# Performance work log

Measured on AMD Instinct MI355X. Metric: run time of the kernel, lower is better.

## Reference

```python
import jax, jax.numpy as jnp
import numpy as np

M, K = 8192, 4096
N_INT4, N_INT8 = 8192, 2816
N_TOTAL = N_INT4 + N_INT8


def setup_inputs() -> dict:
    key = jax.random.key(0)
    k1, k2, k3, k4, k5 = jax.random.split(key, 5)
    x = jax.random.normal(k1, (M, K), dtype=jnp.float32)
    # Precomputed dequantized weight buffers (what forward() actually consumes).
    # Scaled down ~1/sqrt(K) to keep activations O(1), mimicking dequantized int4/int8 weights.
    w_int4_deq = jax.random.normal(k2, (N_INT4, K), dtype=jnp.float32) * 0.02
    w_int8_deq = jax.random.normal(k3, (N_INT8, K), dtype=jnp.float32) * 0.02
    # inv_perm: random permutation mapping concatenated [int4|int8] channels back to original order
    inv_perm = jax.random.permutation(k4, N_TOTAL).astype(jnp.int64)
    bias = jax.random.normal(k5, (N_TOTAL,), dtype=jnp.float32)
    return {"x": x, "w_int4_deq": w_int4_deq, "w_int8_deq": w_int8_deq,
            "inv_perm": inv_perm, "bias": bias}


def reference(x, w_int4_deq, w_int8_deq, inv_perm, bias):
    # Two GEMMs on dequantized weight groups: y = x @ W^T
    y_int4 = jnp.einsum('mk,nk->mn', x, w_int4_deq)   # [M, N_int4]
    y_int8 = jnp.einsum('mk,nk->mn', x, w_int8_deq)   # [M, N_int8]
    y = jnp.concatenate([y_int4, y_int8], axis=-1)    # [M, N_total]
    # Output-channel permutation back to original layout, then bias add
    y = jnp.take(y, inv_perm, axis=-1) + bias
    return y
```

## Files before the change

### kernel.cpp

```cpp
#include <hip/hip_runtime.h>
#include <hip/hip_bf16.h>

#define M_DIM 8192
#define K_DIM 4096
#define N4    8192
#define N8    2816
#define NT    11008
#define TM    (M_DIM / 256)
#define TN    (NT / 256)
#define NKT   (K_DIM / 64)

typedef __attribute__((ext_vector_type(4))) float  f32x4;
typedef __attribute__((ext_vector_type(4))) float  float4v;
typedef __attribute__((ext_vector_type(8))) __bf16 bf16x8;
typedef __attribute__((ext_vector_type(4))) unsigned short ushort4v;
typedef __attribute__((ext_vector_type(8))) unsigned short ushort8v;

__device__ __forceinline__ unsigned short f2bf(float f) {
  union { float f; unsigned int u; } v; v.f = f;
  unsigned int u = v.u;
  unsigned int r = u + 0x7FFFu + ((u >> 16) & 1u);
  return (unsigned short)(r >> 16);
}

__global__ void conv_x_kernel(const float* __restrict__ x,
                              unsigned short* __restrict__ xb, int n8) {
  int idx = blockIdx.x * blockDim.x + threadIdx.x;
  int stride = gridDim.x * blockDim.x;
  for (int i = idx; i < n8; i += stride) {
    const float4v* src = (const float4v*)(x + (size_t)i * 8);
    float4v a = src[0], b = src[1];
    ushort8v o;
    o[0] = f2bf(a[0]); o[1] = f2bf(a[1]); o[2] = f2bf(a[2]); o[3] = f2bf(a[3]);
    o[4] = f2bf(b[0]); o[5] = f2bf(b[1]); o[6] = f2bf(b[2]); o[7] = f2bf(b[3]);
    ((ushort8v*)xb)[i] = o;
  }
}

__global__ void conv_w_kernel(const float* __restrict__ w4,
                              const float* __restrict__ w8,
                              const int* __restrict__ inv_perm,
                              unsigned short* __restrict__ wb) {
  int j = blockIdx.x;
  int c = inv_perm[j];
  const float* src = (c < N4) ? (w4 + (size_t)c * K_DIM)
                              : (w8 + (size_t)(c - N4) * K_DIM);
  unsigned short* dst = wb + (size_t)j * K_DIM;
  int t = threadIdx.x;
#pragma unroll
  for (int it = 0; it < 4; ++it) {
    int e = it * 1024 + t * 4;
    float4v a = *(const float4v*)(src + e);
    ushort4v o;
    o[0] = f2bf(a[0]); o[1] = f2bf(a[1]); o[2] = f2bf(a[2]); o[3] = f2bf(a[3]);
    *(ushort4v*)(dst + e) = o;
  }
}

__global__ __launch_bounds__(512, 2)
void gemm256_kernel(const unsigned short* __restrict__ A,
                    const unsigned short* __restrict__ B,
                    const float* __restrict__ bias,
                    float* __restrict__ C) {
  __shared__ __align__(16) unsigned short lds[4 * 16384];

  int bid = blockIdx.x;
  int wgid = (bid & 7) * ((TM * TN) / 8) + (bid >> 3);
  int tile_m = wgid / TN;
  int tile_n = wgid % TN;

  const int tid  = threadIdx.x;
  const int wid  = tid >> 6;
  const int lane = tid & 63;
  const int wr  = wid >> 2;
  const int wcn = wid & 3;
  const int l15 = lane & 15;
  const int rswz  = (lane & 7) << 4;
  const int coff0 = (((lane >> 4) * 16) + 0)  ^ rswz;
  const int coff1 = (((lane >> 4) * 16) + 64) ^ rswz;
  const int st_row8 = lane >> 3;
  const int st_scol = ((lane & 7) * 16) ^ ((lane & 0x38) << 1);

  const size_t arow0 = (size_t)tile_m * 256;
  const size_t brow0 = (size_t)tile_n * 256;

  auto stage = [&](const unsigned short* __restrict__ g, size_t grow0,
                   unsigned short* ltile, int q, int ktelem) {
    int row = q * 64 + wid * 8 + st_row8;
    const unsigned short* src =
        g + (grow0 + (size_t)row) * K_DIM + ktelem + (st_scol >> 1);
    unsigned short* dst = ltile + (q * 64 + wid * 8) * 64;
    __builtin_amdgcn_global_load_lds(
        (const __attribute__((address_space(1))) void*)src,
        (__attribute__((address_space(3))) void*)dst, 16, 0, 0);
  };
  auto fragld = [&](const unsigned short* ltile, int row, int coff) -> bf16x8 {
    return *(const bf16x8*)((const char*)ltile + row * 128 + coff);
  };

  f32x4 acc[8][4];
#pragma unroll
  for (int i = 0; i < 8; ++i)
#pragma unroll
    for (int j = 0; j < 4; ++j) acc[i][j] = (f32x4){0.f, 0.f, 0.f, 0.f};

  bf16x8 b0[2][2];


  stage(A, arow0, lds + 0,     0, 0);  stage(A, arow0, lds + 0,     2, 0);
  stage(A, arow0, lds + 0,     1, 0);  stage(A, arow0, lds + 0,     3, 0);
  stage(B, brow0, lds + 16384, 0, 0);  stage(B, brow0, lds + 16384, 1, 0);
  stage(B, brow0, lds + 16384, 2, 0);  stage(B, brow0, lds + 16384, 3, 0);
  stage(A, arow0, lds + 32768, 0, 64); stage(A, arow0, lds + 32768, 2, 64);
  stage(B, brow0, lds + 49152, 0, 64); stage(B, brow0, lds + 49152, 1, 64);
  stage(B, brow0, lds + 49152, 2, 64); stage(B, brow0, lds + 49152, 3, 64);
  asm volatile("s_waitcnt vmcnt(6)" ::: "memory");
  __builtin_amdgcn_s_barrier();

#pragma unroll
  for (int n = 0; n < 2; ++n) {
    int row = wcn * 64 + n * 16 + l15;
    b0[n][0] = fragld(lds + 16384, row, coff0);
    b0[n][1] = fragld(lds + 16384, row, coff1);
  }

#define KITER(AC, BC, AN, UN1, UN2)                                           \
  {                                                                           \
    unsigned short* const Ac = (AC);                                          \
    unsigned short* const Bc = (BC);                                          \
    unsigned short* const An = (AN);                                          \
    const int un1 = (UN1);                                                    \
    const int un2 = (UN2);                                                    \
    bf16x8 a0[4][2], a1[4][2], b1[2][2];                                      \
                \
    _Pragma("unroll")                                                         \
    for (int m = 0; m < 4; ++m) {                                             \
      int row = wr * 128 + m * 16 + l15;                                      \
      a0[m][0] = fragld(Ac, row, coff0);                                      \
      a0[m][1] = fragld(Ac, row, coff1);                                      \
    }                                                                         \
    stage(A, arow0, An, 1, un1);                                              \
    stage(A, arow0, An, 3, un1);                                              \
    __builtin_amdgcn_s_barrier();                                             \
    asm volatile("s_waitcnt lgkmcnt(0)" ::: "memory");                        \
    __builtin_amdgcn_sched_barrier(0);                                        \
    __builtin_amdgcn_s_setprio(1);                                            \
    _Pragma("unroll")                                                         \
    for (int m = 0; m < 4; ++m)                                               \
      _Pragma("unroll")                                                       \
      for (int n = 0; n < 2; ++n) {                                           \
        acc[m][n] = __builtin_amdgcn_mfma_f32_16x16x32_bf16(a0[m][0], b0[n][0], acc[m][n], 0, 0, 0); \
        acc[m][n] = __builtin_amdgcn_mfma_f32_16x16x32_bf16(a0[m][1], b0[n][1], acc[m][n], 0, 0, 0); \
      }                                                                       \
    __builtin_amdgcn_s_setprio(0);                                            \
    __builtin_amdgcn_s_barrier();                                             \
     \
    _Pragma("unroll")                                                         \
    for (int n = 0; n < 2; ++n) {                                             \
      int row = wcn * 64 + (2 + n) * 16 + l15;                                \
      b1[n][0] = fragld(Bc, row, coff0);                                      \
      b1[n][1] = fragld(Bc, row, coff1);                                      \
    }                                                                         \
    stage(A, arow0, Ac, 0, un2);                                              \
    stage(A, arow0, Ac, 2, un2);                                              \
    __builtin_amdgcn_s_barrier();                                             \
    asm volatile("s_waitcnt lgkmcnt(0)" ::: "memory");                        \
    __builtin_amdgcn_sched_barrier(0);                                        \
    __builtin_amdgcn_s_setprio(1);                                            \
    _Pragma("unroll")                                                         \
    for (int m = 0; m < 4; ++m)                                               \
      _Pragma("unroll")                                                       \
      for (int n = 0; n < 2; ++n) {                                           \
        acc[m][2 + n] = __builtin_amdgcn_mfma_f32_16x16x32_bf16(a0[m][0], b1[n][0], acc[m][2 + n], 0, 0, 0); \
        acc[m][2 + n] = __builtin_amdgcn_mfma_f32_16x16x32_bf16(a0[m][1], b1[n][1], acc[m][2 + n], 0, 0, 0); \
      }                                                                       \
    __builtin_amdgcn_s_setprio(0);                                            \
    asm volatile("s_waitcnt vmcnt(10)" ::: "memory");      \
    __builtin_amdgcn_s_barrier();                                             \
            \
    _Pragma("unroll")                                                         \
    for (int m = 0; m < 4; ++m) {                                             \
      int row = wr * 128 + 64 + m * 16 + l15;                                 \
      a1[m][0] = fragld(Ac, row, coff0);                                      \
      a1[m][1] = fragld(Ac, row, coff1);                                      \
    }                                                                         \
    stage(B, brow0, Bc, 0, un2);                                              \
    stage(B, brow0, Bc, 1, un2);                                              \
    __builtin_amdgcn_s_barrier();                                             \
    asm volatile("s_waitcnt lgkmcnt(0)" ::: "memory");                        \
    __builtin_amdgcn_sched_barrier(0);                                        \
    __builtin_amdgcn_s_setprio(1);                                            \
    _Pragma("unroll")                                                         \
    for (int m = 0; m < 4; ++m)                                               \
      _Pragma("unroll")                                                       \
      for (int n = 0; n < 2; ++n) {                                           \
        acc[4 + m][n] = __builtin_amdgcn_mfma_f32_16x16x32_bf16(a1[m][0], b0[n][0], acc[4 + m][n], 0, 0, 0); \
        acc[4 + m][n] = __builtin_amdgcn_mfma_f32_16x16x32_bf16(a1[m][1], b0[n][1], acc[4 + m][n], 0, 0, 0); \
      }                                                                       \
    __builtin_amdgcn_s_setprio(0);                                            \
    __builtin_amdgcn_s_barrier();                                             \
                             \
    stage(B, brow0, Bc, 2, un2);                                              \
    stage(B, brow0, Bc, 3, un2);                                              \
    asm volatile("s_waitcnt vmcnt(8)" ::: "memory");                          \
    __builtin_amdgcn_s_barrier();                                             \
    _Pragma("unroll")                                                         \
    for (int n = 0; n < 2; ++n) {                                             \
      int row = wcn * 64 + n * 16 + l15;                                      \
      b0[n][0] = fragld(An + 16384, row, coff0);                              \
      b0[n][1] = fragld(An + 16384, row, coff1);                              \
    }                                                                         \
    __builtin_amdgcn_s_setprio(1);                                            \
    _Pragma("unroll")                                                         \
    for (int m = 0; m < 4; ++m)                                               \
      _Pragma("unroll")                                                       \
      for (int n = 0; n < 2; ++n) {                                           \
        acc[4 + m][2 + n] = __builtin_amdgcn_mfma_f32_16x16x32_bf16(a1[m][0], b1[n][0], acc[4 + m][2 + n], 0, 0, 0); \
        acc[4 + m][2 + n] = __builtin_amdgcn_mfma_f32_16x16x32_bf16(a1[m][1], b1[n][1], acc[4 + m][2 + n], 0, 0, 0); \
      }                                                                       \
    __builtin_amdgcn_s_setprio(0);                                            \
    __builtin_amdgcn_s_barrier();                                             \
  }

#pragma unroll 1
  for (int u = 0; u < NKT; u += 2) {
    const int k1 = ((u + 1 < NKT) ? (u + 1) : (NKT - 1)) * 64;
    const int k2 = ((u + 2 < NKT) ? (u + 2) : (NKT - 1)) * 64;
    const int k3 = ((u + 3 < NKT) ? (u + 3) : (NKT - 1)) * 64;
    KITER(lds + 0,     lds + 16384, lds + 32768, k1, k2);
    KITER(lds + 32768, lds + 49152, lds + 0,     k2, k3);
  }
#undef KITER

#pragma unroll
  for (int n = 0; n < 4; ++n) {
    int col = tile_n * 256 + wcn * 64 + n * 16 + l15;
    float bv = bias[col];
#pragma unroll
    for (int m = 0; m < 8; ++m) {
      int row0 = tile_m * 256 + wr * 128 + m * 16 + ((lane >> 4) * 4);
#pragma unroll
      for (int r = 0; r < 4; ++r) {
        C[(size_t)(row0 + r) * NT + col] = acc[m][n][r] + bv;
      }
    }
  }
}

__global__ void gemm_fused_f32_kernel(const float* __restrict__ x,
                                      const float* __restrict__ w4,
                                      const float* __restrict__ w8,
                                      const int* __restrict__ inv_perm,
                                      const float* __restrict__ bias,
                                      float* __restrict__ C) {
  __shared__ __align__(16) unsigned short Alds[128 * 64];
  __shared__ __align__(16) unsigned short Blds[128 * 64];

  int bid = blockIdx.x;
  int wgid = (bid & 7) * ((M_DIM / 128) * (NT / 128) / 8) + (bid >> 3);
  int tile_n = wgid % (NT / 128);
  int tile_m = wgid / (NT / 128);

  const int tid  = threadIdx.x;
  const int wid  = tid >> 6;
  const int lane = tid & 63;
  const int wr = wid >> 1, wc = wid & 1;

  f32x4 acc[4][4];
#pragma unroll
  for (int i = 0; i < 4; ++i)
#pragma unroll
    for (int j = 0; j < 4; ++j) acc[i][j] = (f32x4){0.f, 0.f, 0.f, 0.f};

  const int lrow = lane >> 3;
  const int lcol = (lane & 7) * 8;

  const float* asrc[4];
  const float* bsrc[4];
  int ldsoff[4];
#pragma unroll
  for (int s = 0; s < 4; ++s) {
    int rb = s * 32 + wid * 8 + lrow;
    asrc[s] = x + (size_t)(tile_m * 128 + rb) * K_DIM + lcol;
    int c = inv_perm[tile_n * 128 + rb];
    bsrc[s] = ((c < N4) ? (w4 + (size_t)c * K_DIM)
                        : (w8 + (size_t)(c - N4) * K_DIM)) + lcol;
    ldsoff[s] = rb * 64 + lcol;
  }

  for (int kt = 0; kt < K_DIM; kt += 64) {
#pragma unroll
    for (int s = 0; s < 4; ++s) {
      float4v a0 = *(const float4v*)(asrc[s] + kt);
      float4v a1 = *(const float4v*)(asrc[s] + kt + 4);
      float4v b0 = *(const float4v*)(bsrc[s] + kt);
      float4v b1 = *(const float4v*)(bsrc[s] + kt + 4);
      ushort8v oa, ob;
      oa[0]=f2bf(a0[0]); oa[1]=f2bf(a0[1]); oa[2]=f2bf(a0[2]); oa[3]=f2bf(a0[3]);
      oa[4]=f2bf(a1[0]); oa[5]=f2bf(a1[1]); oa[6]=f2bf(a1[2]); oa[7]=f2bf(a1[3]);
      ob[0]=f2bf(b0[0]); ob[1]=f2bf(b0[1]); ob[2]=f2bf(b0[2]); ob[3]=f2bf(b0[3]);
      ob[4]=f2bf(b1[0]); ob[5]=f2bf(b1[1]); ob[6]=f2bf(b1[2]); ob[7]=f2bf(b1[3]);
      *(ushort8v*)&Alds[ldsoff[s]] = oa;
      *(ushort8v*)&Blds[ldsoff[s]] = ob;
    }
    __syncthreads();

#pragma unroll
    for (int kk = 0; kk < 2; ++kk) {
      bf16x8 af[4], bfr[4];
#pragma unroll
      for (int i = 0; i < 4; ++i) {
        int row = wr * 64 + i * 16 + (lane & 15);
        af[i] = *(const bf16x8*)&Alds[row * 64 + kk * 32 + (lane >> 4) * 8];
      }
#pragma unroll
      for (int j = 0; j < 4; ++j) {
        int row = wc * 64 + j * 16 + (lane & 15);
        bfr[j] = *(const bf16x8*)&Blds[row * 64 + kk * 32 + (lane >> 4) * 8];
      }
#pragma unroll
      for (int i = 0; i < 4; ++i)
#pragma unroll
        for (int j = 0; j < 4; ++j)
          acc[i][j] = __builtin_amdgcn_mfma_f32_16x16x32_bf16(af[i], bfr[j], acc[i][j], 0, 0, 0);
    }
    __syncthreads();
  }

#pragma unroll
  for (int j = 0; j < 4; ++j) {
    int col = tile_n * 128 + wc * 64 + j * 16 + (lane & 15);
    float bv = bias[col];
#pragma unroll
    for (int i = 0; i < 4; ++i) {
      int row0 = tile_m * 128 + wr * 64 + i * 16 + ((lane >> 4) * 4);
#pragma unroll
      for (int r = 0; r < 4; ++r) {
        C[(size_t)(row0 + r) * NT + col] = acc[i][j][r] + bv;
      }
    }
  }
}

extern "C" void kernel_launch(void* const* d_in, const int* in_sizes, int n_in,
                              void* d_out, int out_size, void* d_ws, size_t ws_size,
                              hipStream_t stream) {
  const float* x    = (const float*)d_in[0];
  const float* w4   = (const float*)d_in[1];
  const float* w8   = (const float*)d_in[2];
  const int*   perm = (const int*)d_in[3];
  const float* bias = (const float*)d_in[4];
  float*       out  = (float*)d_out;

  const size_t xb_bytes = (size_t)M_DIM * K_DIM * 2;
  const size_t wb_bytes = (size_t)NT * K_DIM * 2;

  if (ws_size >= xb_bytes + wb_bytes) {
    unsigned short* xb = (unsigned short*)d_ws;
    unsigned short* wb = xb + (size_t)M_DIM * K_DIM;
    conv_x_kernel<<<2048, 256, 0, stream>>>(x, xb, (M_DIM * K_DIM) / 8);
    conv_w_kernel<<<NT, 256, 0, stream>>>(w4, w8, perm, wb);
    gemm256_kernel<<<TM * TN, 512, 0, stream>>>(xb, wb, bias, out);
  } else {
    int grid = (M_DIM / 128) * (NT / 128);
    gemm_fused_f32_kernel<<<grid, 256, 0, stream>>>(x, w4, w8, perm, bias, out);
  }
}
```

Measured before the change: 739.2 us.

## Split tail-wave GEMM tiles into half-M blocks to balance the last wave

The GEMM has 32*43=1376 tiles of 256x256. The first 1280 tiles keep the full-size path, and the remaining 96 tiles are each split into two 128-row blocks, giving 1472 workgroups. The goal is to reduce tail-wave imbalance across the CUs. The half blocks use a simpler double-buffered loop that waits on vmcnt(0) every iteration, so they pipeline less well and reload each B tile twice.

```diff
diff --git a/kernel.cpp b/kernel.cpp
--- a/kernel.cpp
+++ b/kernel.cpp
@@ -9,6 +9,8 @@
 #define TM    (M_DIM / 256)
 #define TN    (NT / 256)
 #define NKT   (K_DIM / 64)
+#define NFULL 1280
+#define GRID  1472
 
 typedef __attribute__((ext_vector_type(4))) float  f32x4;
 typedef __attribute__((ext_vector_type(4))) float  float4v;
@@ -65,7 +67,10 @@
   __shared__ __align__(16) unsigned short lds[4 * 16384];
 
   int bid = blockIdx.x;
-  int wgid = (bid & 7) * ((TM * TN) / 8) + (bid >> 3);
+  int vbid, mhalf, is_half;
+  if (bid < NFULL) { vbid = bid; mhalf = 0; is_half = 0; }
+  else { int h = bid - NFULL; vbid = NFULL + (h >> 1); mhalf = h & 1; is_half = 1; }
+  int wgid = (vbid & 7) * ((TM * TN) / 8) + (vbid >> 3);
   int tile_m = wgid / TN;
   int tile_n = wgid % TN;
 
@@ -81,7 +86,6 @@
   const int st_row8 = lane >> 3;
   const int st_scol = ((lane & 7) * 16) ^ ((lane & 0x38) << 1);
 
-  const size_t arow0 = (size_t)tile_m * 256;
   const size_t brow0 = (size_t)tile_n * 256;
 
   auto stage = [&](const unsigned short* __restrict__ g, size_t grow0,
@@ -98,6 +102,77 @@
     return *(const bf16x8*)((const char*)ltile + row * 128 + coff);
   };
 
+  if (is_half) {
+    const size_t arowh = (size_t)tile_m * 256 + (size_t)mhalf * 128;
+    f32x4 acch[4][4];
+#pragma unroll
+    for (int i = 0; i < 4; ++i)
+#pragma unroll
+      for (int j = 0; j < 4; ++j) acch[i][j] = (f32x4){0.f, 0.f, 0.f, 0.f};
+
+    stage(A, arowh, lds + 0, 0, 0);      stage(A, arowh, lds + 0, 1, 0);
+    stage(B, brow0, lds + 16384, 0, 0);  stage(B, brow0, lds + 16384, 1, 0);
+    stage(B, brow0, lds + 16384, 2, 0);  stage(B, brow0, lds + 16384, 3, 0);
+    asm volatile("s_waitcnt vmcnt(0)" ::: "memory");
+    __builtin_amdgcn_s_barrier();
+
+#pragma unroll 1
+    for (int u = 0; u < NKT; ++u) {
+      unsigned short* Ac = lds + (u & 1) * 32768;
+      unsigned short* Bc = Ac + 16384;
+      unsigned short* An = lds + (32768 - (u & 1) * 32768);
+      if (u + 1 < NKT) {
+        int kn = (u + 1) * 64;
+        stage(A, arowh, An, 0, kn);      stage(A, arowh, An, 1, kn);
+        stage(B, brow0, An + 16384, 0, kn); stage(B, brow0, An + 16384, 1, kn);
+        stage(B, brow0, An + 16384, 2, kn); stage(B, brow0, An + 16384, 3, kn);
+      }
+      bf16x8 ah[4][2], bh[4][2];
+#pragma unroll
+      for (int m = 0; m < 4; ++m) {
+        int row = wr * 64 + m * 16 + l15;
+        ah[m][0] = fragld(Ac, row, coff0);
+        ah[m][1] = fragld(Ac, row, coff1);
+      }
+#pragma unroll
+      for (int n = 0; n < 4; ++n) {
+        int row = wcn * 64 + n * 16 + l15;
+        bh[n][0] = fragld(Bc, row, coff0);
+        bh[n][1] = fragld(Bc, row, coff1);
+      }
+      asm volatile("s_waitcnt lgkmcnt(0)" ::: "memory");
+      __builtin_amdgcn_sched_barrier(0);
+      __builtin_amdgcn_s_setprio(1);
+#pragma unroll
+      for (int m = 0; m < 4; ++m)
+#pragma unroll
+        for (int n = 0; n < 4; ++n) {
+          acch[m][n] = __builtin_amdgcn_mfma_f32_16x16x32_bf16(ah[m][0], bh[n][0], acch[m][n], 0, 0, 0);
+          acch[m][n] = __builtin_amdgcn_mfma_f32_16x16x32_bf16(ah[m][1], bh[n][1], acch[m][n], 0, 0, 0);
+        }
+      __builtin_amdgcn_s_setprio(0);
+      asm volatile("s_waitcnt vmcnt(0)" ::: "memory");
+      __builtin_amdgcn_s_barrier();
+    }
+
+#pragma unroll
+    for (int n = 0; n < 4; ++n) {
+      int col = tile_n * 256 + wcn * 64 + n * 16 + l15;
+      float bv = bias[col];
+#pragma unroll
+      for (int m = 0; m < 4; ++m) {
+        int row0 = tile_m * 256 + mhalf * 128 + wr * 64 + m * 16 + ((lane >> 4) * 4);
+#pragma unroll
+        for (int r = 0; r < 4; ++r) {
+          C[(size_t)(row0 + r) * NT + col] = acch[m][n][r] + bv;
+        }
+      }
+    }
+    return;
+  }
+
+  const size_t arow0 = (size_t)tile_m * 256;
+
   f32x4 acc[8][4];
 #pragma unroll
   for (int i = 0; i < 8; ++i)
@@ -105,7 +180,6 @@
     for (int j = 0; j < 4; ++j) acc[i][j] = (f32x4){0.f, 0.f, 0.f, 0.f};
 
   bf16x8 b0[2][2];
-
 
   stage(A, arow0, lds + 0,     0, 0);  stage(A, arow0, lds + 0,     2, 0);
   stage(A, arow0, lds + 0,     1, 0);  stage(A, arow0, lds + 0,     3, 0);
@@ -360,7 +434,7 @@
     unsigned short* wb = xb + (size_t)M_DIM * K_DIM;
     conv_x_kernel<<<2048, 256, 0, stream>>>(x, xb, (M_DIM * K_DIM) / 8);
     conv_w_kernel<<<NT, 256, 0, stream>>>(w4, w8, perm, wb);
-    gemm256_kernel<<<TM * TN, 512, 0, stream>>>(xb, wb, bias, out);
+    gemm256_kernel<<<GRID, 512, 0, stream>>>(xb, wb, bias, out);
   } else {
     int grid = (M_DIM / 128) * (NT / 128);
     gemm_fused_f32_kernel<<<grid, 256, 0, stream>>>(x, w4, w8, perm, bias, out);
```

Measured after the change: 731.2 us. No clear change (-1.1%).
